# Optimization experiments

Measured on AMD Instinct MI355X. Metric: run time of the kernel, lower is better.

Reference implementation:

```python
import jax, jax.numpy as jnp
import numpy as np

N_HEADS = 4
N_HIDDEN = 64  # out_features // n_heads
NEG_SLOPE = 0.2


def setup_inputs() -> dict:
    key = jax.random.key(0)
    k1, k2, k3, k4, k5 = jax.random.split(key, 5)
    B, N, F_IN, F_OUT = 1, 4096, 128, 256
    h = jax.random.normal(k1, (B, N, F_IN), dtype=jnp.float32)
    adj_mat = jax.random.uniform(k2, (N, N, 1), dtype=jnp.float32)
    W_proj = jax.random.normal(k3, (F_IN, N_HEADS * N_HIDDEN), dtype=jnp.float32) / np.sqrt(F_IN)
    W_proj_attn = jax.random.normal(k4, (F_IN, N_HEADS * N_HIDDEN // 2), dtype=jnp.float32) / np.sqrt(F_IN)
    w_attn = jax.random.normal(k5, (N_HIDDEN,), dtype=jnp.float32) / np.sqrt(N_HIDDEN)
    return {"h": h, "adj_mat": adj_mat, "W_proj": W_proj, "W_proj_attn": W_proj_attn, "w_attn": w_attn}


def reference(h, adj_mat, W_proj, W_proj_attn, w_attn):
    B, N, _ = h.shape
    H, D = N_HEADS, N_HIDDEN
    half = D // 2
    # value projection: (B, N, H, D)
    g = (h @ W_proj).reshape(B, N, H, D)
    # attention-feature projection: (B, N, H, D//2)
    ga = (h @ W_proj_attn).reshape(B, N, H, half)
    # attn(cat([ga_i, ga_j])) decomposes linearly: e_ij = <w_l, ga_i> + <w_r, ga_j>
    # (identical math to the torch repeat/cat/Linear, without the NxNxD tensor)
    el = jnp.einsum('bnhk,k->bnh', ga, w_attn[:half])   # dest node i term
    er = jnp.einsum('bnhk,k->bnh', ga, w_attn[half:])   # source node j term
    e = jax.nn.leaky_relu(el[:, :, None, :] + er[:, None, :, :], NEG_SLOPE)  # (B, N, N, H)
    mask = adj_mat >= 0.5  # (N, N, 1) broadcasts over (B, N, N, H)
    e = jnp.where(mask, e, -jnp.inf)
    a = jax.nn.softmax(e, axis=2)  # softmax over source nodes j
    # dropout is identity in eval mode
    out = jnp.einsum('bijh,bjhf->bihf', a, g)  # (B, N, H, D)
    return out.reshape(B, N, H * D)  # is_concat=True
```

## Files before the change

kernel.cpp:

```cpp
#include <hip/hip_runtime.h>
#include <hip/hip_bf16.h>

typedef __bf16 bf16_t;
typedef __bf16 bf16x4 __attribute__((ext_vector_type(4)));
typedef __bf16 bf16x8 __attribute__((ext_vector_type(8)));
typedef float floatx4 __attribute__((ext_vector_type(4)));

#define N_NODES 4096
#define F_IN 128
#define NUM_HEADS 4
#define D_HID 64
#define F_OUT 256
#define NEG_SLOPE 0.2f
#define LOG2E 1.4426950408889634f

__global__ __launch_bounds__(384) void proj_kernel(
    const float* __restrict__ hmat, const float* __restrict__ Wp,
    const float* __restrict__ Wa, const float* __restrict__ wattn,
    bf16_t* __restrict__ GB, float* __restrict__ el, float* __restrict__ er)
{
    const int t = threadIdx.x;
    const int j0 = blockIdx.x * 4;

    float acc[4] = {0.f, 0.f, 0.f, 0.f};

    const float* wptr;
    int stride;
    if (t < 256) { wptr = Wp + t;         stride = 256; }
    else         { wptr = Wa + (t - 256); stride = 128; }

    const float* hbase = hmat + (size_t)j0 * F_IN;

    for (int m = 0; m < F_IN; m += 4) {
        const float w0 = wptr[(size_t)(m + 0) * stride];
        const float w1 = wptr[(size_t)(m + 1) * stride];
        const float w2 = wptr[(size_t)(m + 2) * stride];
        const float w3 = wptr[(size_t)(m + 3) * stride];
#pragma unroll
        for (int jl = 0; jl < 4; ++jl) {
            const float4 hv = *reinterpret_cast<const float4*>(&hbase[jl * F_IN + m]);
            acc[jl] = fmaf(hv.w, w3, fmaf(hv.z, w2, fmaf(hv.y, w1, fmaf(hv.x, w0, acc[jl]))));
        }
    }

    if (t < 256) {
        const int h = t >> 6, f = t & 63;
        bf16x4 o;
#pragma unroll
        for (int q = 0; q < 4; ++q) o[q] = (bf16_t)acc[q];
        const size_t base = ((((size_t)h * 128 + (j0 >> 5)) * 4 + (f >> 4)) * 64
                             + (f & 15) + 16 * ((j0 >> 3) & 3)) * 8 + (j0 & 7);
        *reinterpret_cast<bf16x4*>(&GB[base]) = o;
    } else {
        const int ta = t - 256;
        const int ha = ta >> 5, k = ta & 31;
        const float wl = wattn[k] * LOG2E, wr = wattn[32 + k] * LOG2E;
#pragma unroll
        for (int jl = 0; jl < 4; ++jl) {
            float vl = acc[jl] * wl;
            float vr = acc[jl] * wr;
#pragma unroll
            for (int s = 16; s >= 1; s >>= 1) {
                vl += __shfl_xor(vl, s, 64);
                vr += __shfl_xor(vr, s, 64);
            }
            if (k == 0) {
                el[ha * N_NODES + j0 + jl] = vl;
                er[ha * N_NODES + j0 + jl] = vr;
            }
        }
    }
}

__global__ __launch_bounds__(256, 4) void attn_kernel(
    const float* __restrict__ adj, const bf16_t* __restrict__ GB,
    const float* __restrict__ el, const float* __restrict__ er,
    float* __restrict__ numout, float* __restrict__ den_g,
    int njc, int ntiles)
{
    const int tid  = threadIdx.x;
    const int i0   = blockIdx.x * 32;
    const int jc   = blockIdx.y;
    const int jT0  = jc * ntiles * 64;
    const int hh   = tid >> 6;
    const int lane = tid & 63;
    const int m    = lane & 15;
    const int quad = lane >> 4;

    const float el_lo = el[hh * N_NODES + i0 + m];
    const float el_hi = el[hh * N_NODES + i0 + 16 + m];
    const float* adj_lo = adj + (size_t)(i0 + m) * N_NODES;
    const float* adj_hi = adj_lo + (size_t)16 * N_NODES;
    const float* erp    = er + hh * N_NODES;
    const bf16_t* gb_h  = GB + (size_t)hh * (128 * 4 * 512) + lane * 8;

    floatx4 accL0 = {0.f, 0.f, 0.f, 0.f};
    floatx4 accL1 = accL0, accL2 = accL0, accL3 = accL0, accdL = accL0;
    floatx4 accH0 = accL0, accH1 = accL0, accH2 = accL0, accH3 = accL0, accdH = accL0;
    bf16x8 ones;
#pragma unroll
    for (int q = 0; q < 8; ++q) ones[q] = (bf16_t)1.0f;

    for (int k = 0; k < ntiles; ++k) {
        const int jT = jT0 + k * 64;
#pragma unroll
        for (int kt = 0; kt < 2; ++kt) {
            const int jb = jT + kt * 32 + quad * 8;
            const float4 aL0 = *reinterpret_cast<const float4*>(adj_lo + jb);
            const float4 aL1 = *reinterpret_cast<const float4*>(adj_lo + jb + 4);
            const float4 aH0 = *reinterpret_cast<const float4*>(adj_hi + jb);
            const float4 aH1 = *reinterpret_cast<const float4*>(adj_hi + jb + 4);
            const float4 e0  = *reinterpret_cast<const float4*>(erp + jb);
            const float4 e1  = *reinterpret_cast<const float4*>(erp + jb + 4);
            const bf16_t* gp = gb_h + (size_t)((jT >> 5) + kt) * (4 * 512);
            const bf16x8 b0 = *reinterpret_cast<const bf16x8*>(gp);
            const bf16x8 b1 = *reinterpret_cast<const bf16x8*>(gp + 512);
            const bf16x8 b2 = *reinterpret_cast<const bf16x8*>(gp + 1024);
            const bf16x8 b3 = *reinterpret_cast<const bf16x8*>(gp + 1536);

            const float ev[8]  = {e0.x, e0.y, e0.z, e0.w, e1.x, e1.y, e1.z, e1.w};
            const float avL[8] = {aL0.x, aL0.y, aL0.z, aL0.w, aL1.x, aL1.y, aL1.z, aL1.w};
            const float avH[8] = {aH0.x, aH0.y, aH0.z, aH0.w, aH1.x, aH1.y, aH1.z, aH1.w};

            bf16x8 afL, afH;
#pragma unroll
            for (int q = 0; q < 8; ++q) {
                const float sL = el_lo + ev[q];
                const float sH = el_hi + ev[q];
                const float pL = __builtin_amdgcn_exp2f(fmaxf(sL, NEG_SLOPE * sL));
                const float pH = __builtin_amdgcn_exp2f(fmaxf(sH, NEG_SLOPE * sH));
                afL[q] = (bf16_t)(avL[q] >= 0.5f ? pL : 0.0f);
                afH[q] = (bf16_t)(avH[q] >= 0.5f ? pH : 0.0f);
            }

            accdL = __builtin_amdgcn_mfma_f32_16x16x32_bf16(afL, ones, accdL, 0, 0, 0);
            accdH = __builtin_amdgcn_mfma_f32_16x16x32_bf16(afH, ones, accdH, 0, 0, 0);
            accL0 = __builtin_amdgcn_mfma_f32_16x16x32_bf16(afL, b0, accL0, 0, 0, 0);
            accH0 = __builtin_amdgcn_mfma_f32_16x16x32_bf16(afH, b0, accH0, 0, 0, 0);
            accL1 = __builtin_amdgcn_mfma_f32_16x16x32_bf16(afL, b1, accL1, 0, 0, 0);
            accH1 = __builtin_amdgcn_mfma_f32_16x16x32_bf16(afH, b1, accH1, 0, 0, 0);
            accL2 = __builtin_amdgcn_mfma_f32_16x16x32_bf16(afL, b2, accL2, 0, 0, 0);
            accH2 = __builtin_amdgcn_mfma_f32_16x16x32_bf16(afH, b2, accH2, 0, 0, 0);
            accL3 = __builtin_amdgcn_mfma_f32_16x16x32_bf16(afL, b3, accL3, 0, 0, 0);
            accH3 = __builtin_amdgcn_mfma_f32_16x16x32_bf16(afH, b3, accH3, 0, 0, 0);
        }
    }

    float* nrow = numout + (size_t)jc * ((size_t)N_NODES * F_OUT);
    const int ibL = i0 + quad * 4;
    const int ibH = ibL + 16;
#pragma unroll
    for (int r = 0; r < 4; ++r) {
        float* dL = nrow + (size_t)(ibL + r) * F_OUT + hh * D_HID + m;
        dL[0]  = accL0[r];
        dL[16] = accL1[r];
        dL[32] = accL2[r];
        dL[48] = accL3[r];
        float* dH = nrow + (size_t)(ibH + r) * F_OUT + hh * D_HID + m;
        dH[0]  = accH0[r];
        dH[16] = accH1[r];
        dH[32] = accH2[r];
        dH[48] = accH3[r];
    }
    if (m == 0) {
#pragma unroll
        for (int r = 0; r < 4; ++r) {
            den_g[((size_t)jc * N_NODES + ibL + r) * NUM_HEADS + hh] = accdL[r];
            den_g[((size_t)jc * N_NODES + ibH + r) * NUM_HEADS + hh] = accdH[r];
        }
    }
}

template<int NJC>
__global__ __launch_bounds__(256) void reduce_kernel(
    const float* __restrict__ num, const float* __restrict__ den,
    float* __restrict__ out)
{
    const int idx = blockIdx.x * 256 + threadIdx.x;
    const int i  = idx >> 8;
    const int c  = idx & 255;
    const int hh = c >> 6;
    float n = 0.f, d = 0.f;
#pragma unroll
    for (int jc = 0; jc < NJC; ++jc) {
        n += num[(size_t)jc * ((size_t)N_NODES * F_OUT) + idx];
        d += den[((size_t)jc * N_NODES + i) * NUM_HEADS + hh];
    }
    out[idx] = n / d;
}

extern "C" void kernel_launch(void* const* d_in, const int* in_sizes, int n_in,
                              void* d_out, int out_size, void* d_ws, size_t ws_size,
                              hipStream_t stream)
{
    const float* hmat = (const float*)d_in[0];
    const float* adj  = (const float*)d_in[1];
    const float* Wp   = (const float*)d_in[2];
    const float* Wa   = (const float*)d_in[3];
    const float* watt = (const float*)d_in[4];
    float* out = (float*)d_out;

    char* ws = (char*)d_ws;
    bf16_t* GB = (bf16_t*)ws;
    float*  el = (float*)(ws + (2ull << 20));
    float*  er = (float*)(ws + (2ull << 20) + (64ull << 10));
    const size_t baseoff = (2ull << 20) + (128ull << 10);

    const size_t num_bytes = (size_t)N_NODES * F_OUT * 4;
    const size_t den_bytes = (size_t)N_NODES * NUM_HEADS * 4;
    const int njc = (ws_size >= baseoff + 8 * (num_bytes + den_bytes)) ? 8
                  : (ws_size >= baseoff + 4 * (num_bytes + den_bytes)) ? 4 : 2;

    float* num = (float*)(ws + baseoff);
    float* den = (float*)(ws + baseoff + (size_t)njc * num_bytes);

    proj_kernel<<<1024, 384, 0, stream>>>(hmat, Wp, Wa, watt, GB, el, er);
    attn_kernel<<<dim3(128, njc), 256, 0, stream>>>(adj, GB, el, er, num, den,
                                                    njc, (N_NODES / njc) / 64);
    if (njc == 8)      reduce_kernel<8><<<(N_NODES * F_OUT) / 256, 256, 0, stream>>>(num, den, out);
    else if (njc == 4) reduce_kernel<4><<<(N_NODES * F_OUT) / 256, 256, 0, stream>>>(num, den, out);
    else               reduce_kernel<2><<<(N_NODES * F_OUT) / 256, 256, 0, stream>>>(num, den, out);
}
```

Before: 165.8 us.

## Pack adjacency into bitmask, prefetch next tile in attention, vectorize reduce

Adds a mask kernel that compresses the fp32 adjacency matrix into one bit per edge. The attention kernel then reads 32-bit mask words instead of float adjacency values, and its loop is restructured to software-prefetch the next 32-column slice of mask, er and G. The reduce kernel now handles four outputs per thread with float4 loads and a reciprocal multiply. The full 64 MB adjacency is still read once per call in the new launch, so the saving depends on the attention kernel having re-read it or having stalled on load latency.

```diff
diff --git a/kernel.cpp b/kernel.cpp
--- a/kernel.cpp
+++ b/kernel.cpp
@@ -5,6 +5,7 @@
 typedef __bf16 bf16x4 __attribute__((ext_vector_type(4)));
 typedef __bf16 bf16x8 __attribute__((ext_vector_type(8)));
 typedef float floatx4 __attribute__((ext_vector_type(4)));
+typedef unsigned int u32;
 
 #define N_NODES 4096
 #define F_IN 128
@@ -13,6 +14,24 @@
 #define F_OUT 256
 #define NEG_SLOPE 0.2f
 #define LOG2E 1.4426950408889634f
+#define NWORDS 128
+
+__global__ __launch_bounds__(256) void mask_kernel(
+    const float* __restrict__ adj, u32* __restrict__ maskw)
+{
+    const int w = blockIdx.x * 256 + threadIdx.x;
+    const float* src = adj + (size_t)w * 32;
+    u32 bits = 0;
+#pragma unroll
+    for (int c = 0; c < 8; ++c) {
+        const float4 v = *reinterpret_cast<const float4*>(src + c * 4);
+        bits |= (u32)(v.x >= 0.5f) << (4 * c + 0);
+        bits |= (u32)(v.y >= 0.5f) << (4 * c + 1);
+        bits |= (u32)(v.z >= 0.5f) << (4 * c + 2);
+        bits |= (u32)(v.w >= 0.5f) << (4 * c + 3);
+    }
+    maskw[w] = bits;
+}
 
 __global__ __launch_bounds__(384) void proj_kernel(
     const float* __restrict__ hmat, const float* __restrict__ Wp,
@@ -73,26 +92,27 @@
 }
 
 __global__ __launch_bounds__(256, 4) void attn_kernel(
-    const float* __restrict__ adj, const bf16_t* __restrict__ GB,
+    const u32* __restrict__ maskw, const bf16_t* __restrict__ GB,
     const float* __restrict__ el, const float* __restrict__ er,
     float* __restrict__ numout, float* __restrict__ den_g,
-    int njc, int ntiles)
+    int ntiles)
 {
     const int tid  = threadIdx.x;
     const int i0   = blockIdx.x * 32;
     const int jc   = blockIdx.y;
-    const int jT0  = jc * ntiles * 64;
     const int hh   = tid >> 6;
     const int lane = tid & 63;
     const int m    = lane & 15;
     const int quad = lane >> 4;
+    const int NS   = ntiles * 2;
+    const int j32_0 = (jc * ntiles * 64) >> 5;
 
     const float el_lo = el[hh * N_NODES + i0 + m];
     const float el_hi = el[hh * N_NODES + i0 + 16 + m];
-    const float* adj_lo = adj + (size_t)(i0 + m) * N_NODES;
-    const float* adj_hi = adj_lo + (size_t)16 * N_NODES;
-    const float* erp    = er + hh * N_NODES;
-    const bf16_t* gb_h  = GB + (size_t)hh * (128 * 4 * 512) + lane * 8;
+    const u32* mrowL = maskw + (size_t)(i0 + m) * NWORDS;
+    const u32* mrowH = mrowL + (size_t)16 * NWORDS;
+    const float* erp = er + hh * N_NODES + quad * 8;
+    const bf16_t* gb = GB + (size_t)hh * (128 * 4 * 512) + lane * 8;
 
     floatx4 accL0 = {0.f, 0.f, 0.f, 0.f};
     floatx4 accL1 = accL0, accL2 = accL0, accL3 = accL0, accdL = accL0;
@@ -101,49 +121,56 @@
 #pragma unroll
     for (int q = 0; q < 8; ++q) ones[q] = (bf16_t)1.0f;
 
-    for (int k = 0; k < ntiles; ++k) {
-        const int jT = jT0 + k * 64;
-#pragma unroll
-        for (int kt = 0; kt < 2; ++kt) {
-            const int jb = jT + kt * 32 + quad * 8;
-            const float4 aL0 = *reinterpret_cast<const float4*>(adj_lo + jb);
-            const float4 aL1 = *reinterpret_cast<const float4*>(adj_lo + jb + 4);
-            const float4 aH0 = *reinterpret_cast<const float4*>(adj_hi + jb);
-            const float4 aH1 = *reinterpret_cast<const float4*>(adj_hi + jb + 4);
-            const float4 e0  = *reinterpret_cast<const float4*>(erp + jb);
-            const float4 e1  = *reinterpret_cast<const float4*>(erp + jb + 4);
-            const bf16_t* gp = gb_h + (size_t)((jT >> 5) + kt) * (4 * 512);
-            const bf16x8 b0 = *reinterpret_cast<const bf16x8*>(gp);
-            const bf16x8 b1 = *reinterpret_cast<const bf16x8*>(gp + 512);
-            const bf16x8 b2 = *reinterpret_cast<const bf16x8*>(gp + 1024);
-            const bf16x8 b3 = *reinterpret_cast<const bf16x8*>(gp + 1536);
-
-            const float ev[8]  = {e0.x, e0.y, e0.z, e0.w, e1.x, e1.y, e1.z, e1.w};
-            const float avL[8] = {aL0.x, aL0.y, aL0.z, aL0.w, aL1.x, aL1.y, aL1.z, aL1.w};
-            const float avH[8] = {aH0.x, aH0.y, aH0.z, aH0.w, aH1.x, aH1.y, aH1.z, aH1.w};
-
-            bf16x8 afL, afH;
-#pragma unroll
-            for (int q = 0; q < 8; ++q) {
-                const float sL = el_lo + ev[q];
-                const float sH = el_hi + ev[q];
-                const float pL = __builtin_amdgcn_exp2f(fmaxf(sL, NEG_SLOPE * sL));
-                const float pH = __builtin_amdgcn_exp2f(fmaxf(sH, NEG_SLOPE * sH));
-                afL[q] = (bf16_t)(avL[q] >= 0.5f ? pL : 0.0f);
-                afH[q] = (bf16_t)(avH[q] >= 0.5f ? pH : 0.0f);
-            }
-
-            accdL = __builtin_amdgcn_mfma_f32_16x16x32_bf16(afL, ones, accdL, 0, 0, 0);
-            accdH = __builtin_amdgcn_mfma_f32_16x16x32_bf16(afH, ones, accdH, 0, 0, 0);
-            accL0 = __builtin_amdgcn_mfma_f32_16x16x32_bf16(afL, b0, accL0, 0, 0, 0);
-            accH0 = __builtin_amdgcn_mfma_f32_16x16x32_bf16(afH, b0, accH0, 0, 0, 0);
-            accL1 = __builtin_amdgcn_mfma_f32_16x16x32_bf16(afL, b1, accL1, 0, 0, 0);
-            accH1 = __builtin_amdgcn_mfma_f32_16x16x32_bf16(afH, b1, accH1, 0, 0, 0);
-            accL2 = __builtin_amdgcn_mfma_f32_16x16x32_bf16(afL, b2, accL2, 0, 0, 0);
-            accH2 = __builtin_amdgcn_mfma_f32_16x16x32_bf16(afH, b2, accH2, 0, 0, 0);
-            accL3 = __builtin_amdgcn_mfma_f32_16x16x32_bf16(afL, b3, accL3, 0, 0, 0);
-            accH3 = __builtin_amdgcn_mfma_f32_16x16x32_bf16(afH, b3, accH3, 0, 0, 0);
-        }
+    u32 mLc = mrowL[j32_0], mHc = mrowH[j32_0];
+    float4 e0c = *reinterpret_cast<const float4*>(erp + j32_0 * 32);
+    float4 e1c = *reinterpret_cast<const float4*>(erp + j32_0 * 32 + 4);
+    const bf16_t* gp0 = gb + (size_t)j32_0 * 2048;
+    bf16x8 b0c = *reinterpret_cast<const bf16x8*>(gp0);
+    bf16x8 b1c = *reinterpret_cast<const bf16x8*>(gp0 + 512);
+    bf16x8 b2c = *reinterpret_cast<const bf16x8*>(gp0 + 1024);
+    bf16x8 b3c = *reinterpret_cast<const bf16x8*>(gp0 + 1536);
+
+    for (int s = 0; s < NS; ++s) {
+        u32 mLn = 0, mHn = 0;
+        float4 e0n = {0.f, 0.f, 0.f, 0.f}, e1n = e0n;
+        bf16x8 b0n = {}, b1n = {}, b2n = {}, b3n = {};
+        if (s + 1 < NS) {
+            const int jn = j32_0 + s + 1;
+            mLn = mrowL[jn];
+            mHn = mrowH[jn];
+            e0n = *reinterpret_cast<const float4*>(erp + jn * 32);
+            e1n = *reinterpret_cast<const float4*>(erp + jn * 32 + 4);
+            const bf16_t* gp = gb + (size_t)jn * 2048;
+            b0n = *reinterpret_cast<const bf16x8*>(gp);
+            b1n = *reinterpret_cast<const bf16x8*>(gp + 512);
+            b2n = *reinterpret_cast<const bf16x8*>(gp + 1024);
+            b3n = *reinterpret_cast<const bf16x8*>(gp + 1536);
+        }
+        const u32 byL = (mLc >> (quad * 8)) & 0xff;
+        const u32 byH = (mHc >> (quad * 8)) & 0xff;
+        const float ev[8] = {e0c.x, e0c.y, e0c.z, e0c.w, e1c.x, e1c.y, e1c.z, e1c.w};
+        bf16x8 afL, afH;
+#pragma unroll
+        for (int q = 0; q < 8; ++q) {
+            const float sL = el_lo + ev[q];
+            const float sH = el_hi + ev[q];
+            const float pL = __builtin_amdgcn_exp2f(fmaxf(sL, NEG_SLOPE * sL));
+            const float pH = __builtin_amdgcn_exp2f(fmaxf(sH, NEG_SLOPE * sH));
+            afL[q] = (bf16_t)(((byL >> q) & 1u) ? pL : 0.0f);
+            afH[q] = (bf16_t)(((byH >> q) & 1u) ? pH : 0.0f);
+        }
+        accdL = __builtin_amdgcn_mfma_f32_16x16x32_bf16(afL, ones, accdL, 0, 0, 0);
+        accdH = __builtin_amdgcn_mfma_f32_16x16x32_bf16(afH, ones, accdH, 0, 0, 0);
+        accL0 = __builtin_amdgcn_mfma_f32_16x16x32_bf16(afL, b0c, accL0, 0, 0, 0);
+        accH0 = __builtin_amdgcn_mfma_f32_16x16x32_bf16(afH, b0c, accH0, 0, 0, 0);
+        accL1 = __builtin_amdgcn_mfma_f32_16x16x32_bf16(afL, b1c, accL1, 0, 0, 0);
+        accH1 = __builtin_amdgcn_mfma_f32_16x16x32_bf16(afH, b1c, accH1, 0, 0, 0);
+        accL2 = __builtin_amdgcn_mfma_f32_16x16x32_bf16(afL, b2c, accL2, 0, 0, 0);
+        accH2 = __builtin_amdgcn_mfma_f32_16x16x32_bf16(afH, b2c, accH2, 0, 0, 0);
+        accL3 = __builtin_amdgcn_mfma_f32_16x16x32_bf16(afL, b3c, accL3, 0, 0, 0);
+        accH3 = __builtin_amdgcn_mfma_f32_16x16x32_bf16(afH, b3c, accH3, 0, 0, 0);
+        mLc = mLn; mHc = mHn; e0c = e0n; e1c = e1n;
+        b0c = b0n; b1c = b1n; b2c = b2n; b3c = b3n;
     }
 
     float* nrow = numout + (size_t)jc * ((size_t)N_NODES * F_OUT);
@@ -176,17 +203,22 @@
     const float* __restrict__ num, const float* __restrict__ den,
     float* __restrict__ out)
 {
-    const int idx = blockIdx.x * 256 + threadIdx.x;
-    const int i  = idx >> 8;
-    const int c  = idx & 255;
-    const int hh = c >> 6;
-    float n = 0.f, d = 0.f;
+    const int t4   = blockIdx.x * 256 + threadIdx.x;
+    const int base = t4 * 4;
+    const int i  = base >> 8;
+    const int hh = (base & 255) >> 6;
+    float4 n = {0.f, 0.f, 0.f, 0.f};
+    float d = 0.f;
 #pragma unroll
     for (int jc = 0; jc < NJC; ++jc) {
-        n += num[(size_t)jc * ((size_t)N_NODES * F_OUT) + idx];
+        const float4 v = *reinterpret_cast<const float4*>(
+            num + (size_t)jc * ((size_t)N_NODES * F_OUT) + base);
+        n.x += v.x; n.y += v.y; n.z += v.z; n.w += v.w;
         d += den[((size_t)jc * N_NODES + i) * NUM_HEADS + hh];
     }
-    out[idx] = n / d;
+    const float rd = 1.0f / d;
+    float4 o = {n.x * rd, n.y * rd, n.z * rd, n.w * rd};
+    *reinterpret_cast<float4*>(out + base) = o;
 }
 
 extern "C" void kernel_launch(void* const* d_in, const int* in_sizes, int n_in,
@@ -201,10 +233,11 @@
     float* out = (float*)d_out;
 
     char* ws = (char*)d_ws;
-    bf16_t* GB = (bf16_t*)ws;
-    float*  el = (float*)(ws + (2ull << 20));
-    float*  er = (float*)(ws + (2ull << 20) + (64ull << 10));
-    const size_t baseoff = (2ull << 20) + (128ull << 10);
+    bf16_t* GB   = (bf16_t*)ws;
+    float*  el   = (float*)(ws + (2ull << 20));
+    float*  er   = (float*)(ws + (2ull << 20) + (64ull << 10));
+    u32*    mskw = (u32*)(ws + (2ull << 20) + (128ull << 10));
+    const size_t baseoff = (4ull << 20) + (128ull << 10);
 
     const size_t num_bytes = (size_t)N_NODES * F_OUT * 4;
     const size_t den_bytes = (size_t)N_NODES * NUM_HEADS * 4;
@@ -215,9 +248,10 @@
     float* den = (float*)(ws + baseoff + (size_t)njc * num_bytes);
 
     proj_kernel<<<1024, 384, 0, stream>>>(hmat, Wp, Wa, watt, GB, el, er);
-    attn_kernel<<<dim3(128, njc), 256, 0, stream>>>(adj, GB, el, er, num, den,
-                                                    njc, (N_NODES / njc) / 64);
-    if (njc == 8)      reduce_kernel<8><<<(N_NODES * F_OUT) / 256, 256, 0, stream>>>(num, den, out);
-    else if (njc == 4) reduce_kernel<4><<<(N_NODES * F_OUT) / 256, 256, 0, stream>>>(num, den, out);
-    else               reduce_kernel<2><<<(N_NODES * F_OUT) / 256, 256, 0, stream>>>(num, den, out);
-}
+    mask_kernel<<<(N_NODES * NWORDS) / 256, 256, 0, stream>>>(adj, mskw);
+    attn_kernel<<<dim3(128, njc), 256, 0, stream>>>(mskw, GB, el, er, num, den,
+                                                    (N_NODES / njc) / 64);
+    if (njc == 8)      reduce_kernel<8><<<(N_NODES * F_OUT) / 1024, 256, 0, stream>>>(num, den, out);
+    else if (njc == 4) reduce_kernel<4><<<(N_NODES * F_OUT) / 1024, 256, 0, stream>>>(num, den, out);
+    else               reduce_kernel<2><<<(N_NODES * F_OUT) / 1024, 256, 0, stream>>>(num, den, out);
+}
```

Result: faster. 159.9 us (-3.6%).
